# Performance work log

Measured on AMD Instinct MI355X. Metric: run time of the kernel, lower is better.

## Reference

```python
import jax, jax.numpy as jnp
import numpy as np

NUM_ROUTED = 256
DIM = 2048
TOPK = 8
ROUTE_SCALE = 2.5


def setup_inputs() -> dict:
    key = jax.random.key(0)
    k_x, k_w = jax.random.split(key)
    x = jax.random.normal(k_x, (4, 4096, DIM), dtype=jnp.float32)
    # nn.Parameter(torch.empty) -> treat as learned weight; init small normal
    weight = jax.random.normal(k_w, (NUM_ROUTED, DIM), dtype=jnp.float32) * 0.02
    bias = jnp.zeros((NUM_ROUTED,), dtype=jnp.float32)
    return {"x": x, "weight": weight, "bias": bias}


def reference(x, weight, bias):
    # logits: [b, s, e]
    logits = jnp.einsum("bsd,ed->bse", x, weight)
    scores = jax.nn.sigmoid(logits)
    scores_for_selection = scores + bias  # bias only affects selection
    _, indices = jax.lax.top_k(scores_for_selection, TOPK)  # [b, s, k]
    weights = jnp.take_along_axis(scores, indices, axis=-1)  # gather original scores
    weights = weights / (jnp.sum(weights, axis=-1, keepdims=True) + 1e-20)
    weights = weights * ROUTE_SCALE
    return weights, indices
```

## Files before the change

### kernel.cpp

```cpp
#include <hip/hip_runtime.h>
#include <math.h>
#include <limits.h>

#define DIM 2048
#define NEXP 256
#define TOPK 8
#define BM 32
#define BK 16
#define NTH 512
#define NTILE 128


typedef float f32x2 __attribute__((ext_vector_type(2)));

__device__ __forceinline__ f32x2 pkmul(f32x2 a, f32x2 b) {
    f32x2 d;
    asm("v_pk_mul_f32 %0, %1, %2" : "=v"(d) : "v"(a), "v"(b));
    return d;
}
__device__ __forceinline__ f32x2 pkadd(f32x2 a, f32x2 b) {
    f32x2 d;
    asm("v_pk_add_f32 %0, %1, %2" : "=v"(d) : "v"(a), "v"(b));
    return d;
}

__device__ __forceinline__ void gload16(const void* gptr, void* lptr) {
    __builtin_amdgcn_global_load_lds(
        (const __attribute__((address_space(1))) unsigned int*)(unsigned long long)gptr,
        (__attribute__((address_space(3))) unsigned int*)(unsigned int)(unsigned long long)lptr,
        16, 0, 0);
}

__global__ __launch_bounds__(NTH) void gate_kernel(
    const float* __restrict__ x, const float* __restrict__ w,
    const float* __restrict__ bias, float* __restrict__ outw,
    float* __restrict__ outi)
{
#pragma clang fp contract(off)
    __shared__ float wbuf[2][4096];
    __shared__ float xbuf[2][512];

    const int tid   = threadIdx.x;
    const int elane = tid & 63;
    const int r0    = (tid >> 6) * 4;
    const int gr    = blockIdx.x * BM;

    const int we    = tid & 255;
    const int chalf = tid >> 8;
    const char* wbase = (const char*)w + (size_t)we * (DIM * 4);
    const int xrow = tid >> 2, xq = tid & 3;
    const char* xbase = (const char*)x + ((size_t)(gr + xrow) * DIM + xq * 4) * 4;

    auto stage = [&](int buf, int kt) {
        const size_t kb = (size_t)kt * 64;
        char* dst = (char*)&wbuf[buf][0] + we * 16;
        const int c0 = chalf * 2;
        gload16(wbase + kb + c0 * 16,        dst + c0 * 4096);
        gload16(wbase + kb + (c0 + 1) * 16,  dst + (c0 + 1) * 4096);
        if (tid < 128)
            gload16(xbase + kb, (char*)&xbuf[buf][0] + tid * 16);
    };

    f32x2 acc[4][4][2];
#pragma unroll
    for (int r = 0; r < 4; ++r)
#pragma unroll
        for (int i = 0; i < 4; ++i)
#pragma unroll
            for (int p = 0; p < 2; ++p) acc[r][i][p] = (f32x2){0.0f, 0.0f};

    auto compute = [&](int buf) {
#pragma unroll
        for (int c = 3; c >= 0; --c) {
            f32x2 xlo[4], xhi[4];
#pragma unroll
            for (int r = 0; r < 4; ++r) {
                const float4 xv = *(const float4*)&xbuf[buf][(r0 + r) * BK + c * 4];
                xlo[r] = (f32x2){xv.x, xv.y};
                xhi[r] = (f32x2){xv.z, xv.w};
            }
            __builtin_amdgcn_s_setprio(1);
#pragma unroll
            for (int i = 0; i < 4; ++i) {
                const float4 wv = *(const float4*)&wbuf[buf][(c * 256 + elane + 64 * i) * 4];
                const f32x2 wlo = (f32x2){wv.x, wv.y};
                const f32x2 whi = (f32x2){wv.z, wv.w};
#pragma unroll
                for (int r = 0; r < 4; ++r) {
                    acc[r][i][0] = pkadd(acc[r][i][0], pkmul(xlo[r], wlo));
                    acc[r][i][1] = pkadd(acc[r][i][1], pkmul(xhi[r], whi));
                }
            }
            __builtin_amdgcn_s_setprio(0);
        }
    };

    stage(0, 0);
    __syncthreads();
    for (int kt = 0; kt < NTILE; ++kt) {
        const int buf = kt & 1;
        if (kt + 1 < NTILE) stage(buf ^ 1, kt + 1);
        compute(buf);
        __syncthreads();
    }

    float* sc = &wbuf[0][0];
#pragma unroll
    for (int r = 0; r < 4; ++r)
#pragma unroll
        for (int i = 0; i < 4; ++i) {
            const float l01 = acc[r][i][0].x + acc[r][i][0].y;
            const float l23 = acc[r][i][1].x + acc[r][i][1].y;
            const float logit = l01 + l23;
            const double s = 1.0 / (1.0 + exp(-(double)logit));
            sc[(r0 + r) * NEXP + (elane + 64 * i)] = (float)s;
        }
    __syncthreads();

    float* cval = &xbuf[0][0];
    int*   cidx = (int*)&xbuf[1][0];

    if (tid < 64) {
        const int row = tid >> 1;
        const int sub = tid & 1;
        float tv[TOPK];
        int   ti[TOPK];
#pragma unroll
        for (int q = 0; q < TOPK; ++q) { tv[q] = -INFINITY; ti[q] = INT_MAX; }
        for (int j = 0; j < 128; ++j) {
            const int e = sub + (j << 1);
            const float v = sc[row * NEXP + e] + bias[e];
            if (v > tv[TOPK - 1]) {
                int p = TOPK - 1;
                while (p > 0 && v > tv[p - 1]) {
                    tv[p] = tv[p - 1]; ti[p] = ti[p - 1]; --p;
                }
                tv[p] = v; ti[p] = e;
            }
        }
#pragma unroll
        for (int q = 0; q < TOPK; ++q) {
            cval[row * 16 + sub * 8 + q] = tv[q];
            cidx[row * 16 + sub * 8 + q] = ti[q];
        }
    }
    __syncthreads();

    if (tid < 32) {
        const int row = tid;
        int p0 = 0, p1 = 0;
        float g[TOPK];
        int   sel[TOPK];
#pragma unroll
        for (int k = 0; k < TOPK; ++k) {
            const float v0 = cval[row * 16 + p0];
            const int   i0 = cidx[row * 16 + p0];
            const float v1 = cval[row * 16 + 8 + p1];
            const int   i1 = cidx[row * 16 + 8 + p1];
            int take0;
            if (v0 > v1) take0 = 1;
            else if (v1 > v0) take0 = 0;
            else take0 = (i0 < i1);
            const int e = take0 ? i0 : i1;
            p0 += take0; p1 += 1 - take0;
            sel[k] = e;
            g[k] = sc[row * NEXP + e];
        }
        const float s01 = g[0] + g[1], s23 = g[2] + g[3];
        const float s45 = g[4] + g[5], s67 = g[6] + g[7];
        const float wsum = (s01 + s23) + (s45 + s67);
        const float den = wsum + 1e-20f;
        const size_t orow = (size_t)(gr + row) * TOPK;
#pragma unroll
        for (int k = 0; k < TOPK; ++k) {
            outw[orow + k] = (g[k] / den) * 2.5f;
            outi[orow + k] = (float)sel[k];
        }
    }
}

extern "C" void kernel_launch(void* const* d_in, const int* in_sizes, int n_in,
                              void* d_out, int out_size, void* d_ws, size_t ws_size,
                              hipStream_t stream) {
    const float* x    = (const float*)d_in[0];
    const float* w    = (const float*)d_in[1];
    const float* bias = (const float*)d_in[2];
    float* outw = (float*)d_out;
    const int M = in_sizes[0] / DIM;
    float* outi = outw + (size_t)M * TOPK;
    const int grid = M / BM;
    hipLaunchKernelGGL(gate_kernel, dim3(grid), dim3(NTH), 0, stream,
                       x, w, bias, outw, outi);
}
```

Baseline: 395.3 us.

## Triple-buffer LDS staging with partial vmcnt waits instead of full syncs

Moves the K-loop from double to triple buffering, unrolled by three. Each step waits with `s_waitcnt vmcnt(3)` plus a barrier, so only the oldest tile's async global-to-LDS loads must land while the newer prefetch stays in flight. The x-tile loads are also remapped so each wave loads the rows it will use. The goal is to keep more memory traffic in flight and hide load latency behind compute. The cost is extra LDS (three buffers) and a hand-written wait count that must match the number of loads each lane issues.

```diff
diff --git a/kernel.cpp b/kernel.cpp
--- a/kernel.cpp
+++ b/kernel.cpp
@@ -31,34 +31,39 @@
         16, 0, 0);
 }
 
+#define WAITBAR3() asm volatile("s_waitcnt vmcnt(3)\ns_barrier" ::: "memory")
+
 __global__ __launch_bounds__(NTH) void gate_kernel(
     const float* __restrict__ x, const float* __restrict__ w,
     const float* __restrict__ bias, float* __restrict__ outw,
     float* __restrict__ outi)
 {
 #pragma clang fp contract(off)
-    __shared__ float wbuf[2][4096];
-    __shared__ float xbuf[2][512];
+    __shared__ float wbuf[3][4096];
+    __shared__ float xbuf[3][512];
 
     const int tid   = threadIdx.x;
-    const int elane = tid & 63;
-    const int r0    = (tid >> 6) * 4;
+    const int lane  = tid & 63;
+    const int wid   = tid >> 6;
+    const int elane = lane;
+    const int r0    = wid * 4;
     const int gr    = blockIdx.x * BM;
 
     const int we    = tid & 255;
     const int chalf = tid >> 8;
-    const char* wbase = (const char*)w + (size_t)we * (DIM * 4);
-    const int xrow = tid >> 2, xq = tid & 3;
-    const char* xbase = (const char*)x + ((size_t)(gr + xrow) * DIM + xq * 4) * 4;
-
-    auto stage = [&](int buf, int kt) {
-        const size_t kb = (size_t)kt * 64;
-        char* dst = (char*)&wbuf[buf][0] + we * 16;
-        const int c0 = chalf * 2;
-        gload16(wbase + kb + c0 * 16,        dst + c0 * 4096);
-        gload16(wbase + kb + (c0 + 1) * 16,  dst + (c0 + 1) * 4096);
-        if (tid < 128)
-            gload16(xbase + kb, (char*)&xbuf[buf][0] + tid * 16);
+    const char* wsrc = (const char*)w + (size_t)we * (DIM * 4) + chalf * 32;
+    const unsigned wdoff = we * 16 + chalf * 8192;
+
+    const int xr = r0 + (lane >> 2), xq = lane & 3;
+    const char* xsrc = (const char*)x + ((size_t)(gr + xr) * DIM + xq * 4) * 4;
+    const unsigned xdoff = xr * 64 + xq * 16;
+
+    auto stage = [&](int buf, size_t kb) {
+        char* wd = (char*)&wbuf[buf][0] + wdoff;
+        gload16(wsrc + kb,      wd);
+        gload16(wsrc + kb + 16, wd + 4096);
+        if (lane < 16)
+            gload16(xsrc + kb, (char*)&xbuf[buf][0] + xdoff);
     };
 
     f32x2 acc[4][4][2];
@@ -96,13 +101,19 @@
     };
 
     stage(0, 0);
+    stage(1, 64);
+    WAITBAR3();
+
+    for (int t = 0; t < 126; t += 3) {
+        const size_t kb = (size_t)t * 64;
+        stage(2, kb + 128); compute(0); WAITBAR3();
+        stage(0, kb + 192); compute(1); WAITBAR3();
+        stage(1, kb + 256); compute(2); WAITBAR3();
+    }
+    compute(0);
+    asm volatile("s_waitcnt vmcnt(0)\ns_barrier" ::: "memory");
+    compute(1);
     __syncthreads();
-    for (int kt = 0; kt < NTILE; ++kt) {
-        const int buf = kt & 1;
-        if (kt + 1 < NTILE) stage(buf ^ 1, kt + 1);
-        compute(buf);
-        __syncthreads();
-    }
 
     float* sc = &wbuf[0][0];
 #pragma unroll
```

After: 492.3 us. 24.5% more time.
